# Kernel tuning notes

Measured on AMD Instinct MI355X. Metric: run time of the kernel, lower is better.

## Reference

```python
import jax, jax.numpy as jnp
import numpy as np

N = 20000      # nodes
E = 320000     # edges
IN = 256       # in node feats
EIN = 64       # in edge feats
H = 4          # heads
FO = 64        # out node feats per head (H*FO == IN for residual)
FE = 16        # out edge feats per head
NEG_SLOPE = 0.2


def setup_inputs() -> dict:
    key = jax.random.key(0)
    ks = jax.random.split(key, 10)
    s = 0.05
    return {
        "x": jax.random.normal(ks[0], (N, IN), jnp.float32),
        "efeats": jax.random.normal(ks[1], (E, EIN), jnp.float32),
        "src": jax.random.randint(ks[2], (E,), 0, N),
        "dst": jax.random.randint(ks[3], (E,), 0, N),
        "W_ni": jax.random.normal(ks[4], (IN, H * FE), jnp.float32) * s,
        "W_fij": jax.random.normal(ks[5], (EIN, H * FE), jnp.float32) * s,
        "W_nj": jax.random.normal(ks[6], (IN, H * FE), jnp.float32) * s,
        "W_src": jax.random.normal(ks[7], (IN, H * FO), jnp.float32) * s,
        "attn": jax.random.normal(ks[8], (H, FE), jnp.float32) * s,
        "bias": jnp.zeros((H * FE,), jnp.float32),
    }


def _leaky_relu(x):
    return jnp.where(x >= 0, x, NEG_SLOPE * x)


def reference(x, efeats, src, dst, W_ni, W_fij, W_nj, W_src, attn, bias):
    # --- DGL EGATConv ---
    # edge scores: f_ij = LeakyReLU(W_ni h_src + W_fij e_ij + W_nj h_dst + b)
    f = (x @ W_ni)[src] + efeats @ W_fij + (x @ W_nj)[dst] + bias   # [E, H*FE]
    f = _leaky_relu(f).reshape(E, H, FE)
    e = jnp.einsum('ehf,hf->eh', f, attn)                            # [E, H]
    # edge softmax over edges grouped by destination node
    m = jax.ops.segment_max(e, dst, num_segments=N)                  # [N, H]
    ex = jnp.exp(e - m[dst])
    denom = jax.ops.segment_sum(ex, dst, num_segments=N)             # [N, H]
    a = ex / denom[dst]                                              # [E, H]
    # message passing: sum_j a_ij * (W_src h_j)
    h = (x @ W_src).reshape(N, H, FO)
    msg = a[:, :, None] * h[src]                                     # [E, H, FO]
    hi = jax.ops.segment_sum(msg, dst, num_segments=N).reshape(N, H * FO)
    # --- flatten heads + residual (EGATBaseModule) ---
    out = hi + x
    return out, f.reshape(E, H * FE)
```

## Files before the change

kernel.cpp:

```cpp
#include <hip/hip_runtime.h>

#define N_NODES 20000
#define N_EDGES 320000
#define IN_F 256
#define EIN_F 64
#define NH 4
#define HFE 64
#define HFO 256
#define NCOL 384
#define SLOTS 64

typedef __attribute__((ext_vector_type(8))) short short8;
typedef __attribute__((ext_vector_type(4))) float f32x4;

__device__ inline short f2bf(float f) {
    unsigned u = __builtin_bit_cast(unsigned, f);
    unsigned r = (u + 0x7FFFu + ((u >> 16) & 1u)) >> 16;
    return (short)r;
}
__device__ inline float bf2f(unsigned short u) {
    unsigned v = ((unsigned)u) << 16;
    return __builtin_bit_cast(float, v);
}

__global__ void k_pack(const float* __restrict__ Wni, const float* __restrict__ Wnj,
                       const float* __restrict__ Wsrc, const float* __restrict__ Wfij,
                       short* __restrict__ wpack, short* __restrict__ wfpack) {
    int idx = blockIdx.x * 256 + threadIdx.x;
    if (idx < IN_F * NCOL) {
        int k = idx / NCOL, col = idx % NCOL;
        float v;
        if (col < 64)        v = Wni[k * 64 + col];
        else if (col < 128)  v = Wnj[k * 64 + (col - 64)];
        else                 v = Wsrc[k * 256 + (col - 128)];
        int kb = k >> 5, ct = col >> 4, g = (k >> 3) & 3, i = k & 7, l15 = col & 15;
        wpack[(((kb * 24 + ct) * 64) + g * 16 + l15) * 8 + i] = f2bf(v);
    } else if (idx < IN_F * NCOL + EIN_F * 64) {
        int j = idx - IN_F * NCOL;
        int k = j >> 6, col = j & 63;
        int kb = k >> 5, ct = col >> 4, g = (k >> 3) & 3, i = k & 7, l15 = col & 15;
        wfpack[(((kb * 4 + ct) * 64) + g * 16 + l15) * 8 + i] = f2bf(Wfij[k * 64 + col]);
    }
}

__global__ __launch_bounds__(256) void k1_mfma(
    const float* __restrict__ x, const short* __restrict__ wpack,
    short* __restrict__ xni_b, short* __restrict__ xnj_b, short* __restrict__ hfeat_b,
    int* __restrict__ cur)
{
    const int tid  = threadIdx.x;
    const int w    = tid >> 6;
    const int lane = tid & 63;
    const int l15  = lane & 15;
    const int g    = lane >> 4;

    const int r0 = blockIdx.x * 16;
    if (tid < 16) cur[r0 + tid] = 0;

    f32x4 acc[6];
#pragma unroll
    for (int j = 0; j < 6; j++) acc[j] = (f32x4){0.f, 0.f, 0.f, 0.f};

    const short8* bp = (const short8*)wpack;
    const float* xrow = x + (size_t)(r0 + l15) * 256;

    for (int kb = 0; kb < 8; kb++) {
        const float* ap = xrow + kb * 32 + 8 * g;
        float4 a0 = *(const float4*)ap;
        float4 a1 = *(const float4*)(ap + 4);
        short8 afr;
        afr[0] = f2bf(a0.x); afr[1] = f2bf(a0.y); afr[2] = f2bf(a0.z); afr[3] = f2bf(a0.w);
        afr[4] = f2bf(a1.x); afr[5] = f2bf(a1.y); afr[6] = f2bf(a1.z); afr[7] = f2bf(a1.w);
        const short8* bkb = bp + (size_t)kb * 24 * 64 + lane;
#pragma unroll
        for (int j = 0; j < 6; j++)
            acc[j] = __builtin_amdgcn_mfma_f32_16x16x32_bf16(afr, bkb[(w * 6 + j) * 64], acc[j], 0, 0, 0);
    }

    const int rowb = r0 + 4 * g;
#pragma unroll
    for (int j = 0; j < 6; j++) {
        const int col = (w * 6 + j) * 16 + l15;
#pragma unroll
        for (int reg = 0; reg < 4; reg++) {
            const int row = rowb + reg;
            if (col < 64)        xni_b[(size_t)row * 64 + col] = f2bf(acc[j][reg]);
            else if (col < 128)  xnj_b[(size_t)row * 64 + (col - 64)] = f2bf(acc[j][reg]);
            else                 hfeat_b[(size_t)row * 256 + (col - 128)] = f2bf(acc[j][reg]);
        }
    }
}

__global__ __launch_bounds__(256) void k2_edge_mfma(
    const float* __restrict__ efeats, const int* __restrict__ src, const int* __restrict__ dst,
    const short* __restrict__ wfpack, const float* __restrict__ attn,
    const float* __restrict__ bias,
    const short* __restrict__ xni_b, const short* __restrict__ xnj_b,
    float* __restrict__ fout, float* __restrict__ escore_pad,
    int* __restrict__ srcslot, int* __restrict__ cur)
{
    const int tid  = threadIdx.x;
    const int w    = tid >> 6;
    const int lane = tid & 63;
    const int l15  = lane & 15;
    const int g    = lane >> 4;

    float4 bias4[4], attn4[4];
#pragma unroll
    for (int ct = 0; ct < 4; ct++) {
        bias4[ct] = *(const float4*)(bias + ct * 16 + 4 * g);
        attn4[ct] = *(const float4*)(attn + ct * 16 + 4 * g);
    }

    short8 bfr[2][4];
    const short8* wf = (const short8*)wfpack;
#pragma unroll
    for (int kb = 0; kb < 2; kb++)
#pragma unroll
        for (int ct = 0; ct < 4; ct++)
            bfr[kb][ct] = wf[(kb * 4 + ct) * 64 + lane];

    const int nwaves = gridDim.x * 4;
    const int gwid = blockIdx.x * 4 + w;
    const int ngroups = N_EDGES / 16;

    for (int grp = gwid; grp < ngroups; grp += nwaves) {
        const int e0 = grp * 16;
        const int e  = e0 + l15;

        const int sv = src[e];
        const int dv = dst[e];

        ushort4 xgv[4], ygv[4];
#pragma unroll
        for (int ct = 0; ct < 4; ct++) {
            xgv[ct] = *(const ushort4*)(xni_b + (size_t)sv * 64 + ct * 16 + 4 * g);
            ygv[ct] = *(const ushort4*)(xnj_b + (size_t)dv * 64 + ct * 16 + 4 * g);
        }

        f32x4 c[4];
#pragma unroll
        for (int ct = 0; ct < 4; ct++) c[ct] = (f32x4){0.f, 0.f, 0.f, 0.f};

#pragma unroll
        for (int kb = 0; kb < 2; kb++) {
            const float* ap = efeats + (size_t)e * 64 + kb * 32 + 8 * g;
            float4 a0 = *(const float4*)ap;
            float4 a1 = *(const float4*)(ap + 4);
            short8 afr;
            afr[0] = f2bf(a0.x); afr[1] = f2bf(a0.y); afr[2] = f2bf(a0.z); afr[3] = f2bf(a0.w);
            afr[4] = f2bf(a1.x); afr[5] = f2bf(a1.y); afr[6] = f2bf(a1.z); afr[7] = f2bf(a1.w);
#pragma unroll
            for (int ct = 0; ct < 4; ct++)
                c[ct] = __builtin_amdgcn_mfma_f32_16x16x32_bf16(bfr[kb][ct], afr, c[ct], 0, 0, 0);
        }

        float p[4];
#pragma unroll
        for (int ct = 0; ct < 4; ct++) {
            float4 f4;
            f4.x = c[ct][0] + bf2f(xgv[ct].x) + bf2f(ygv[ct].x) + bias4[ct].x;
            f4.y = c[ct][1] + bf2f(xgv[ct].y) + bf2f(ygv[ct].y) + bias4[ct].y;
            f4.z = c[ct][2] + bf2f(xgv[ct].z) + bf2f(ygv[ct].z) + bias4[ct].z;
            f4.w = c[ct][3] + bf2f(xgv[ct].w) + bf2f(ygv[ct].w) + bias4[ct].w;
            f4.x = (f4.x >= 0.f) ? f4.x : 0.2f * f4.x;
            f4.y = (f4.y >= 0.f) ? f4.y : 0.2f * f4.y;
            f4.z = (f4.z >= 0.f) ? f4.z : 0.2f * f4.z;
            f4.w = (f4.w >= 0.f) ? f4.w : 0.2f * f4.w;
            *(float4*)(fout + (size_t)e * 64 + ct * 16 + 4 * g) = f4;
            p[ct] = f4.x * attn4[ct].x + f4.y * attn4[ct].y
                  + f4.z * attn4[ct].z + f4.w * attn4[ct].w;
        }

#pragma unroll
        for (int ct = 0; ct < 4; ct++) {
            p[ct] += __shfl_xor(p[ct], 16, 64);
            p[ct] += __shfl_xor(p[ct], 32, 64);
        }

        if (g == 0) {
            float4 exv = {__expf(p[0]), __expf(p[1]), __expf(p[2]), __expf(p[3])};
            const int pos = atomicAdd(&cur[dv], 1);
            const size_t slot = ((size_t)dv << 6) + pos;
            *(float4*)(escore_pad + slot * 4) = exv;
            srcslot[slot] = sv;
        }
    }
}

__global__ __launch_bounds__(256) void k5_gather(
    const int* __restrict__ cur, const int* __restrict__ srcslot,
    const float* __restrict__ escore_pad, const short* __restrict__ hfeat_b,
    const float* __restrict__ x, float* __restrict__ out)
{
    const int w = threadIdx.x >> 6, lane = threadIdx.x & 63;
    const int d = blockIdx.x * 4 + w;
    if (d >= N_NODES) return;
    const int deg = cur[d];
    const int h = lane >> 4;
    const int s0 = d << 6;

    const size_t ob = (size_t)d * 256 + lane * 4;
    const float4 xr = *(const float4*)(x + ob);
    if (deg == 0) {
        *(float4*)(out + ob) = xr;
        return;
    }

    float a0 = 0.f, a1 = 0.f, a2 = 0.f, a3 = 0.f, dsum = 0.f;
    for (int base = 0; base < deg; base += 8) {
        const int m = deg - base;
        int sj[8]; float wj[8]; ushort4 hv[8];
#pragma unroll
        for (int j = 0; j < 8; j++) if (j < m) sj[j] = srcslot[s0 + base + j];
#pragma unroll
        for (int j = 0; j < 8; j++) if (j < m)
            wj[j] = escore_pad[(size_t)(s0 + base + j) * 4 + h];
#pragma unroll
        for (int j = 0; j < 8; j++) if (j < m)
            hv[j] = *(const ushort4*)(hfeat_b + (size_t)sj[j] * 256 + lane * 4);
#pragma unroll
        for (int j = 0; j < 8; j++) if (j < m) {
            const float s = wj[j];
            dsum += s;
            a0 += s * bf2f(hv[j].x);
            a1 += s * bf2f(hv[j].y);
            a2 += s * bf2f(hv[j].z);
            a3 += s * bf2f(hv[j].w);
        }
    }

    const float inv = 1.f / dsum;
    float4 o = {xr.x + a0 * inv, xr.y + a1 * inv, xr.z + a2 * inv, xr.w + a3 * inv};
    *(float4*)(out + ob) = o;
}

extern "C" void kernel_launch(void* const* d_in, const int* in_sizes, int n_in,
                              void* d_out, int out_size, void* d_ws, size_t ws_size,
                              hipStream_t stream) {
    const float* x      = (const float*)d_in[0];
    const float* efeats = (const float*)d_in[1];
    const int*   src    = (const int*)d_in[2];
    const int*   dst    = (const int*)d_in[3];
    const float* Wni    = (const float*)d_in[4];
    const float* Wfij   = (const float*)d_in[5];
    const float* Wnj    = (const float*)d_in[6];
    const float* Wsrc   = (const float*)d_in[7];
    const float* attn   = (const float*)d_in[8];
    const float* bias   = (const float*)d_in[9];

    float* out  = (float*)d_out;
    float* fout = out + (size_t)N_NODES * HFO;

    float* ws         = (float*)d_ws;
    float* escore_pad = ws;
    int*   srcslot    = (int*)(escore_pad + (size_t)N_NODES * SLOTS * 4);
    int*   cur        = srcslot + (size_t)N_NODES * SLOTS;
    short* xni_b      = (short*)(cur + N_NODES);
    short* xnj_b      = xni_b + (size_t)N_NODES * 64;
    short* hfeat_b    = xnj_b + (size_t)N_NODES * 64;
    short* wpack      = hfeat_b + (size_t)N_NODES * 256;
    short* wfpack     = wpack + (size_t)IN_F * NCOL;

    k_pack<<<400, 256, 0, stream>>>(Wni, Wnj, Wsrc, Wfij, wpack, wfpack);
    k1_mfma<<<N_NODES / 16, 256, 0, stream>>>(x, wpack, xni_b, xnj_b, hfeat_b, cur);
    k2_edge_mfma<<<640, 256, 0, stream>>>(efeats, src, dst, wfpack, attn, bias,
                                          xni_b, xnj_b, fout, escore_pad, srcslot, cur);
    k5_gather<<<(N_NODES + 3) / 4, 256, 0, stream>>>(cur, srcslot, escore_pad,
                                                     hfeat_b, x, out);
}
```

Baseline: 121.2 us.

## Move destination-slot bucketing into node GEMM kernel as extra blocks

```diff
diff --git a/kernel.cpp b/kernel.cpp
--- a/kernel.cpp
+++ b/kernel.cpp
@@ -25,7 +25,8 @@
 
 __global__ void k_pack(const float* __restrict__ Wni, const float* __restrict__ Wnj,
                        const float* __restrict__ Wsrc, const float* __restrict__ Wfij,
-                       short* __restrict__ wpack, short* __restrict__ wfpack) {
+                       short* __restrict__ wpack, short* __restrict__ wfpack,
+                       int* __restrict__ cur) {
     int idx = blockIdx.x * 256 + threadIdx.x;
     if (idx < IN_F * NCOL) {
         int k = idx / NCOL, col = idx % NCOL;
@@ -41,13 +42,25 @@
         int kb = k >> 5, ct = col >> 4, g = (k >> 3) & 3, i = k & 7, l15 = col & 15;
         wfpack[(((kb * 4 + ct) * 64) + g * 16 + l15) * 8 + i] = f2bf(Wfij[k * 64 + col]);
     }
-}
-
-__global__ __launch_bounds__(256) void k1_mfma(
+    if (idx < N_NODES) cur[idx] = 0;
+}
+
+__global__ __launch_bounds__(256) void k1_fill(
     const float* __restrict__ x, const short* __restrict__ wpack,
     short* __restrict__ xni_b, short* __restrict__ xnj_b, short* __restrict__ hfeat_b,
-    int* __restrict__ cur)
+    const int* __restrict__ src, const int* __restrict__ dst,
+    int* __restrict__ cur, int* __restrict__ srcslot, int* __restrict__ epos)
 {
+    if (blockIdx.x >= 1250) {
+        const int e = (blockIdx.x - 1250) * 256 + threadIdx.x;
+        const int dv = dst[e];
+        const int pos = atomicAdd(&cur[dv], 1);
+        const int slot = (dv << 6) + pos;
+        srcslot[slot] = src[e];
+        epos[e] = slot;
+        return;
+    }
+
     const int tid  = threadIdx.x;
     const int w    = tid >> 6;
     const int lane = tid & 63;
@@ -55,7 +68,6 @@
     const int g    = lane >> 4;
 
     const int r0 = blockIdx.x * 16;
-    if (tid < 16) cur[r0 + tid] = 0;
 
     f32x4 acc[6];
 #pragma unroll
@@ -93,11 +105,10 @@
 
 __global__ __launch_bounds__(256) void k2_edge_mfma(
     const float* __restrict__ efeats, const int* __restrict__ src, const int* __restrict__ dst,
-    const short* __restrict__ wfpack, const float* __restrict__ attn,
-    const float* __restrict__ bias,
+    const int* __restrict__ epos, const short* __restrict__ wfpack,
+    const float* __restrict__ attn, const float* __restrict__ bias,
     const short* __restrict__ xni_b, const short* __restrict__ xnj_b,
-    float* __restrict__ fout, float* __restrict__ escore_pad,
-    int* __restrict__ srcslot, int* __restrict__ cur)
+    float* __restrict__ fout, float* __restrict__ escore_pad)
 {
     const int tid  = threadIdx.x;
     const int w    = tid >> 6;
@@ -130,6 +141,7 @@
 
         const int sv = src[e];
         const int dv = dst[e];
+        const int ep = epos[e];
 
         ushort4 xgv[4], ygv[4];
 #pragma unroll
@@ -180,10 +192,7 @@
 
         if (g == 0) {
             float4 exv = {__expf(p[0]), __expf(p[1]), __expf(p[2]), __expf(p[3])};
-            const int pos = atomicAdd(&cur[dv], 1);
-            const size_t slot = ((size_t)dv << 6) + pos;
-            *(float4*)(escore_pad + slot * 4) = exv;
-            srcslot[slot] = sv;
+            *(float4*)(escore_pad + (size_t)ep * 4) = exv;
         }
     }
 }
@@ -255,17 +264,19 @@
     float* ws         = (float*)d_ws;
     float* escore_pad = ws;
     int*   srcslot    = (int*)(escore_pad + (size_t)N_NODES * SLOTS * 4);
-    int*   cur        = srcslot + (size_t)N_NODES * SLOTS;
+    int*   epos       = srcslot + (size_t)N_NODES * SLOTS;
+    int*   cur        = epos + N_EDGES;
     short* xni_b      = (short*)(cur + N_NODES);
     short* xnj_b      = xni_b + (size_t)N_NODES * 64;
     short* hfeat_b    = xnj_b + (size_t)N_NODES * 64;
     short* wpack      = hfeat_b + (size_t)N_NODES * 256;
     short* wfpack     = wpack + (size_t)IN_F * NCOL;
 
-    k_pack<<<400, 256, 0, stream>>>(Wni, Wnj, Wsrc, Wfij, wpack, wfpack);
-    k1_mfma<<<N_NODES / 16, 256, 0, stream>>>(x, wpack, xni_b, xnj_b, hfeat_b, cur);
-    k2_edge_mfma<<<640, 256, 0, stream>>>(efeats, src, dst, wfpack, attn, bias,
-                                          xni_b, xnj_b, fout, escore_pad, srcslot, cur);
+    k_pack<<<416, 256, 0, stream>>>(Wni, Wnj, Wsrc, Wfij, wpack, wfpack, cur);
+    k1_fill<<<2500, 256, 0, stream>>>(x, wpack, xni_b, xnj_b, hfeat_b,
+                                      src, dst, cur, srcslot, epos);
+    k2_edge_mfma<<<640, 256, 0, stream>>>(efeats, src, dst, epos, wfpack, attn, bias,
+                                          xni_b, xnj_b, fout, escore_pad);
     k5_gather<<<(N_NODES + 3) / 4, 256, 0, stream>>>(cur, srcslot, escore_pad,
                                                      hfeat_b, x, out);
 }
```

Result: slower. 131.4 us (+8.4%).
